# Kernel optimization log

Hardware: AMD Instinct MI355X
Metric: run time of the kernel (lower is better)

Reference implementation:

```python
import jax, jax.numpy as jnp
import numpy as np

N = 100000   # nodes
H = 96       # hidden_dim
A = 32       # attn_dim
De = 16      # edge_embeddings_dim
E = 500000   # edges per edge type
NEG_SLOPE = 0.01  # torch F.leaky_relu default


def setup_inputs() -> dict:
    key = jax.random.key(0)
    ks = jax.random.split(key, 24)
    nrm = lambda k, shape, s=1.0: jax.random.normal(k, shape, dtype=jnp.float32) * s
    idx = lambda k: jax.random.randint(k, (E,), 0, N, dtype=jnp.int32)
    Din = 2 * H + De
    return {
        'h': nrm(ks[0], (N, H)),
        'src0': idx(ks[1]), 'dst0': idx(ks[2]),
        'src1': idx(ks[3]), 'dst1': idx(ks[4]),
        'src2': idx(ks[5]), 'dst2': idx(ks[6]),
        'Wm0': nrm(ks[7], (Din, H), Din ** -0.5), 'bm0': jnp.zeros((H,), jnp.float32), 'ef0': nrm(ks[8], (De,)),
        'Wm1': nrm(ks[9], (Din, H), Din ** -0.5), 'bm1': jnp.zeros((H,), jnp.float32), 'ef1': nrm(ks[10], (De,)),
        'Wm2': nrm(ks[11], (Din, H), Din ** -0.5), 'bm2': jnp.zeros((H,), jnp.float32), 'ef2': nrm(ks[12], (De,)),
        'Wn0': nrm(ks[13], (H, A), H ** -0.5), 'Wa0': nrm(ks[14], (2 * A, 1), (2 * A) ** -0.5),
        'Wn1': nrm(ks[15], (H, A), H ** -0.5), 'Wa1': nrm(ks[16], (2 * A, 1), (2 * A) ** -0.5),
        'Wu': nrm(ks[17], (4 * H, H), (4 * H) ** -0.5), 'bu': jnp.zeros((H,), jnp.float32),
    }


def _leaky(x):
    return jnp.where(x > 0, x, NEG_SLOPE * x)


def _edge_msg(h, src, dst, Wm, bm, ef):
    # cat(src_h, dst_h, edge_feature) -> Linear  (dropout p=0, eval mode)
    x = jnp.concatenate([h[src], h[dst], jnp.broadcast_to(ef, (src.shape[0], ef.shape[0]))], axis=-1)
    return x @ Wm + bm  # [E, H]


def _mean_agg(m, dst):
    # fn.mean('m','msg'): per-destination mean over incoming edges
    s = jax.ops.segment_sum(m, dst, num_segments=N)
    c = jax.ops.segment_sum(jnp.ones((m.shape[0],), m.dtype), dst, num_segments=N)
    return s / jnp.maximum(c, 1.0)[:, None]


def _attn_agg(scores, m, dst):
    # per-destination softmax over mailbox (variable-size), then weighted sum
    smax = jax.ops.segment_max(scores, dst, num_segments=N)
    ex = jnp.exp(scores - smax[dst])
    den = jax.ops.segment_sum(ex, dst, num_segments=N)
    num = jax.ops.segment_sum(ex[:, None] * m, dst, num_segments=N)
    return num / jnp.maximum(den, 1e-9)[:, None]


def reference(h, src0, dst0, src1, dst1, src2, dst2,
              Wm0, bm0, ef0, Wm1, bm1, ef1, Wm2, bm2, ef2,
              Wn0, Wa0, Wn1, Wa1, Wu, bu):
    # edge type 0: intra_diff (attention), type 1: inter_diff (attention), type 2: intra_lt (mean)
    m0 = _edge_msg(h, src0, dst0, Wm0, bm0, ef0)
    m1 = _edge_msg(h, src1, dst1, Wm1, bm1, ef1)
    m2 = _edge_msg(h, src2, dst2, Wm2, bm2, ef2)

    z0 = h @ Wn0  # [N, A]
    s0 = _leaky(jnp.concatenate([z0[src0], z0[dst0]], axis=-1) @ Wa0)[:, 0]  # [E]
    z1 = h @ Wn1
    s1 = _leaky(jnp.concatenate([z1[src1], z1[dst1]], axis=-1) @ Wa1)[:, 0]

    msg0 = _attn_agg(s0, m0, dst0)   # [N, H]
    msg1 = _attn_agg(s1, m1, dst1)
    msg2 = _mean_agg(m2, dst2)

    # cross_reducer='stack' then concat over edge-type dim -> [N, 3H]
    mcat = jnp.concatenate([msg0, msg1, msg2], axis=-1)
    # cell node update: Linear(cat(h, m)) + ReLU
    return jax.nn.relu(jnp.concatenate([h, mcat], axis=-1) @ Wu + bu)
```

## Files before the change

### kernel.cpp

```cpp
#include <hip/hip_runtime.h>
#include <hip/hip_bf16.h>
#include <cstdint>

#define NN 100000
#define HH 96
#define AD 32
#define DE 16
#define EE 500000
#define NEG 0.01f

#define GSH 10
#define GSZ 1024
#define KB 98
#define CH 4096
#define BPT 123

typedef __bf16 bf16x8 __attribute__((ext_vector_type(8)));
typedef float  f32x4  __attribute__((ext_vector_type(4)));

__device__ __forceinline__ unsigned short f2b(float x) {
    union { float f; unsigned int u; } v; v.f = x;
    unsigned int r = v.u + 0x7fffu + ((v.u >> 16) & 1u);
    return (unsigned short)(r >> 16);
}
__device__ __forceinline__ float b2f(unsigned short h) {
    union { unsigned int u; float f; } v; v.u = ((unsigned int)h) << 16;
    return v.f;
}

__global__ void prep_kernel(const float* Wm0, const float* bm0, const float* ef0,
                            const float* Wm1, const float* bm1, const float* ef1,
                            const float* Wm2, const float* bm2, const float* ef2,
                            const float* Wn0, const float* Wa0,
                            const float* Wn1, const float* Wa1,
                            const float* Wu,
                            float* cvec, float* wvec,
                            unsigned short* BfN, unsigned short* BfU) {
    const float* Wm[3] = {Wm0, Wm1, Wm2};
    const float* bm[3] = {bm0, bm1, bm2};
    const float* ef[3] = {ef0, ef1, ef2};
    const int total = 288 + 384 + 55296 + 36864;
    for (int i = blockIdx.x * blockDim.x + threadIdx.x; i < total;
         i += gridDim.x * blockDim.x) {
        if (i < 288) {
            int t = i / 96, j = i % 96;
            float s = bm[t][j];
            for (int k = 0; k < DE; ++k) s += ef[t][k] * Wm[t][(2 * HH + k) * HH + j];
            cvec[i] = s;
        } else if (i < 288 + 384) {
            int ii = i - 288;
            int kind = ii / 96, k = ii % 96;
            const float* Wn = (kind < 2) ? Wn0 : Wn1;
            const float* Wa = (kind < 2) ? Wa0 : Wa1;
            int off = (kind & 1) ? AD : 0;
            float s = 0.f;
            for (int a = 0; a < AD; ++a) s += Wn[k * AD + a] * Wa[off + a];
            wvec[ii] = s;
        } else if (i < 288 + 384 + 55296) {
            int ii = i - 672;
            int sec = ii / 9216; int rem = ii % 9216;
            int ksc = rem / 512; int lj = rem % 512;
            int ks = ksc / 6, c = ksc % 6;
            int lane = lj / 8, jj = lj % 8;
            int quad = lane / 16, m = lane % 16;
            int k = ks * 32 + quad * 8 + jj;
            int n = c * 16 + m;
            int mt = (sec < 3) ? sec : sec - 3;
            int rowoff = (sec < 3) ? 0 : HH;
            BfN[ii] = f2b(Wm[mt][(rowoff + k) * HH + n]);
        } else {
            int ii = i - (672 + 55296);
            int ksc = ii / 512; int lj = ii % 512;
            int ks = ksc / 6, c = ksc % 6;
            int lane = lj / 8, jj = lj % 8;
            int quad = lane / 16, m = lane % 16;
            int k = ks * 32 + quad * 8 + jj;
            int n = c * 16 + m;
            BfU[ii] = f2b(Wu[k * HH + n]);
        }
    }
}

__global__ void cast_uv_kernel(const float* __restrict__ h, const float* __restrict__ wvec,
                               unsigned short* __restrict__ hb, float* __restrict__ uv) {
    int lane = threadIdx.x & 31;
    int node = (blockIdx.x * blockDim.x + threadIdx.x) >> 5;
    if (node >= NN) return;
    float h0 = h[node * HH + lane];
    float h1 = h[node * HH + 32 + lane];
    float h2 = h[node * HH + 64 + lane];
    hb[node * HH + lane] = f2b(h0);
    hb[node * HH + 32 + lane] = f2b(h1);
    hb[node * HH + 64 + lane] = f2b(h2);
    float acc[4];
#pragma unroll
    for (int q = 0; q < 4; ++q)
        acc[q] = h0 * wvec[q * 96 + lane] + h1 * wvec[q * 96 + 32 + lane] +
                 h2 * wvec[q * 96 + 64 + lane];
#pragma unroll
    for (int d = 16; d >= 1; d >>= 1)
#pragma unroll
        for (int q = 0; q < 4; ++q) acc[q] += __shfl_down(acc[q], d, 32);
    if (lane == 0) {
#pragma unroll
        for (int q = 0; q < 4; ++q) uv[q * NN + node] = acc[q];
    }
}

__global__ void zero_kernel(float4* __restrict__ p, int n4) {
    for (int i = blockIdx.x * blockDim.x + threadIdx.x; i < n4;
         i += gridDim.x * blockDim.x)
        p[i] = make_float4(0.f, 0.f, 0.f, 0.f);
}

__global__ void bucket_hist(const int* __restrict__ d0, const int* __restrict__ d1,
                            const int* __restrict__ d2, int* __restrict__ bCnt) {
    __shared__ int hist[3 * KB];
    int t = threadIdx.x;
    for (int j = t; j < 3 * KB; j += 256) hist[j] = 0;
    __syncthreads();
    const int total = 3 * EE;
    for (int i = blockIdx.x * blockDim.x + t; i < total; i += gridDim.x * blockDim.x) {
        int ty = i / EE, e = i - ty * EE;
        const int* d = (ty == 0) ? d0 : (ty == 1) ? d1 : d2;
        atomicAdd(&hist[ty * KB + (d[e] >> GSH)], 1);
    }
    __syncthreads();
    for (int j = t; j < 3 * KB; j += 256)
        if (hist[j]) atomicAdd(&bCnt[j], hist[j]);
}

__global__ void bucket_scan(const int* __restrict__ bCnt, int* __restrict__ bBase,
                            int* __restrict__ gCursor, int* __restrict__ rs) {
    __shared__ int hist[3 * KB];
    int t = threadIdx.x;
    if (t < 3 * KB) hist[t] = bCnt[t];
    __syncthreads();
    if (t < 3) {
        int run = 0;
        for (int b = 0; b < KB; ++b) {
            bBase[t * (KB + 1) + b] = run;
            gCursor[t * KB + b] = run;
            run += hist[t * KB + b];
        }
        bBase[t * (KB + 1) + KB] = run;
        rs[(size_t)t * (NN + 1) + NN] = run;
    }
}

__global__ __launch_bounds__(256) void bucket_scatter(
    const int* __restrict__ s0, const int* __restrict__ d0,
    const int* __restrict__ s1, const int* __restrict__ d1,
    const int* __restrict__ s2, const int* __restrict__ d2,
    int* __restrict__ gCursor, unsigned int* __restrict__ binned) {
    __shared__ unsigned int recs[CH];
    __shared__ unsigned short rnk[CH];
    __shared__ unsigned char bkt[CH];
    __shared__ int cnt[KB];
    __shared__ int gpos[KB];
    int t = threadIdx.x;
    int type = blockIdx.x / BPT;
    int chunk = (blockIdx.x % BPT) * CH;
    const int* src = (type == 0) ? s0 : (type == 1) ? s1 : s2;
    const int* dst = (type == 0) ? d0 : (type == 1) ? d1 : d2;
    if (t < KB) cnt[t] = 0;
    __syncthreads();
#pragma unroll
    for (int k = 0; k < CH / 256; ++k) {
        int idx = k * 256 + t;
        int e = chunk + idx;
        if (e < EE) {
            int s = src[e], d = dst[e];
            int b = d >> GSH;
            recs[idx] = ((unsigned int)s << GSH) | (unsigned int)(d & (GSZ - 1));
            bkt[idx] = (unsigned char)b;
            rnk[idx] = (unsigned short)atomicAdd(&cnt[b], 1);
        } else {
            bkt[idx] = 0xFF;
        }
    }
    __syncthreads();
    if (t < KB) {
        int c = cnt[t];
        gpos[t] = (c > 0) ? atomicAdd(&gCursor[type * KB + t], c) : 0;
    }
    __syncthreads();
    unsigned int* bout = binned + (size_t)type * EE;
#pragma unroll
    for (int k = 0; k < CH / 256; ++k) {
        int idx = k * 256 + t;
        unsigned char b = bkt[idx];
        if (b != 0xFF) bout[gpos[b] + rnk[idx]] = recs[idx];
    }
}

__global__ __launch_bounds__(256) void bucket_sort(
    const unsigned int* __restrict__ binned, const int* __restrict__ bBase,
    int* __restrict__ rs, int* __restrict__ sorted) {
    __shared__ int cnt[GSZ];
    __shared__ int tsum[256];
    int t = threadIdx.x;
    int type = blockIdx.x / KB;
    int b = blockIdx.x % KB;
    int nodeBase = b * GSZ;
    int eb = bBase[type * (KB + 1) + b];
    int en = bBase[type * (KB + 1) + b + 1];
    int n = en - eb;
    const unsigned int* bin = binned + (size_t)type * EE + eb;
#pragma unroll
    for (int k = 0; k < GSZ / 256; ++k) cnt[k * 256 + t] = 0;
    __syncthreads();
    for (int i = t; i < n; i += 256) atomicAdd(&cnt[bin[i] & (GSZ - 1)], 1);
    __syncthreads();
    int v[4], s = 0;
#pragma unroll
    for (int k = 0; k < 4; ++k) { v[k] = cnt[t * 4 + k]; s += v[k]; }
    tsum[t] = s;
    __syncthreads();
    for (int off = 1; off < 256; off <<= 1) {
        int add = (t >= off) ? tsum[t - off] : 0;
        __syncthreads();
        tsum[t] += add;
        __syncthreads();
    }
    int run = tsum[t] - s;
    int offk[4];
#pragma unroll
    for (int k = 0; k < 4; ++k) { offk[k] = run; run += v[k]; }
    int* rsrow = rs + (size_t)type * (NN + 1) + nodeBase;
#pragma unroll
    for (int k = 0; k < 4; ++k) {
        int node = t * 4 + k;
        if (nodeBase + node < NN) rsrow[node] = eb + offk[k];
    }
    __syncthreads();
#pragma unroll
    for (int k = 0; k < 4; ++k) cnt[t * 4 + k] = offk[k];
    __syncthreads();
    int* so = sorted + (size_t)type * EE + eb;
    for (int i = t; i < n; i += 256) {
        unsigned int r = bin[i];
        int dl = r & (GSZ - 1);
        int p = atomicAdd(&cnt[dl], 1);
        so[p] = (int)(r >> GSH);
    }
}

__global__ __launch_bounds__(256) void node_gemm_kernel(const unsigned short* __restrict__ hb,
                                                        const unsigned short* __restrict__ BfN,
                                                        unsigned short* __restrict__ Pall,
                                                        unsigned short* __restrict__ Qall) {
    const size_t NH = (size_t)NN * HH;
    int wave = threadIdx.x >> 6;
    int lane = threadIdx.x & 63;
    int quad = lane >> 4, m = lane & 15;
    int blk = blockIdx.x * 4 + wave;
    if (blk >= NN / 16) return;
    int sec = blockIdx.y;
    unsigned short* dst = (sec < 3) ? (Pall + (size_t)sec * NH)
                                    : (Qall + (size_t)(sec - 3) * NH);
    int r0 = blk * 16;
    f32x4 acc[6] = {};
    const unsigned short* arow = hb + (size_t)(r0 + m) * HH + quad * 8;
#pragma unroll
    for (int ks = 0; ks < 3; ++ks) {
        bf16x8 af = *(const bf16x8*)(arow + ks * 32);
#pragma unroll
        for (int c = 0; c < 6; ++c) {
            bf16x8 bfv = *(const bf16x8*)(BfN + (((sec * 3 + ks) * 6 + c) << 9) + lane * 8);
            acc[c] = __builtin_amdgcn_mfma_f32_16x16x32_bf16(af, bfv, acc[c], 0, 0, 0);
        }
    }
#pragma unroll
    for (int c = 0; c < 6; ++c)
#pragma unroll
        for (int r = 0; r < 4; ++r) {
            int row = r0 + quad * 4 + r;
            dst[(size_t)row * HH + c * 16 + m] = f2b(acc[c][r]);
        }
}

__global__ void aggregate_kernel(const int* __restrict__ rsAll, const int* __restrict__ sortedAll,
                                 const float* __restrict__ uv,
                                 const unsigned short* __restrict__ Pall,
                                 const unsigned short* __restrict__ Qall,
                                 const float* __restrict__ cvec,
                                 unsigned short* __restrict__ msgb) {
    const size_t NH = (size_t)NN * HH;
    int lane = threadIdx.x & 31;
    int node = (blockIdx.x * blockDim.x + threadIdx.x) >> 5;
    if (node >= NN) return;
    int t = blockIdx.y;
    int is_attn = (t < 2);
    const int* rs = rsAll + (size_t)t * (NN + 1);
    const int* sorted = sortedAll + (size_t)t * EE;
    const float* u = uv + 2 * t * NN;
    const unsigned short* P = Pall + (size_t)t * NH;
    const unsigned short* Q = Qall + (size_t)t * NH;
    const float* cvec_t = cvec + t * 96;

    int beg = rs[node], end = rs[node + 1];
    float a0 = 0.f, a1 = 0.f, a2 = 0.f, den = 0.f;
    float vd = is_attn ? uv[(2 * t + 1) * NN + node] : 0.f;
    for (int base = beg; base < end; base += 32) {
        int batch = end - base;
        if (batch > 32) batch = 32;
        int li = lane < batch ? lane : batch - 1;
        int myS = sorted[base + li];
#pragma unroll 1
        for (int j = 0; j < batch; j += 8) {
            int rem = batch - j;
            int sI[8];
            float wv[8];
#pragma unroll
            for (int k = 0; k < 8; ++k) sI[k] = __shfl(myS, (k < rem ? j + k : j), 32);
            if (is_attn) {
#pragma unroll
                for (int k = 0; k < 8; ++k) {
                    float c = u[sI[k]] + vd;
                    c = c > 0.f ? c : NEG * c;
                    wv[k] = __expf(c);
                }
            } else {
#pragma unroll
                for (int k = 0; k < 8; ++k) wv[k] = 1.f;
            }
#pragma unroll
            for (int k = 0; k < 8; ++k) if (k >= rem) wv[k] = 0.f;
            float x0[8], x1[8], x2[8];
#pragma unroll
            for (int k = 0; k < 8; ++k) {
                const unsigned short* pr = P + (size_t)sI[k] * HH;
                x0[k] = b2f(pr[lane]);
                x1[k] = b2f(pr[lane + 32]);
                x2[k] = b2f(pr[lane + 64]);
            }
#pragma unroll
            for (int k = 0; k < 8; ++k) {
                den += wv[k];
                a0 += wv[k] * x0[k];
                a1 += wv[k] * x1[k];
                a2 += wv[k] * x2[k];
            }
        }
    }
    float r0 = 0.f, r1 = 0.f, r2 = 0.f;
    if (den > 0.f) {
        float inv = 1.f / den;
        const unsigned short* qr = Q + (size_t)node * HH;
        r0 = a0 * inv + b2f(qr[lane]) + cvec_t[lane];
        r1 = a1 * inv + b2f(qr[lane + 32]) + cvec_t[lane + 32];
        r2 = a2 * inv + b2f(qr[lane + 64]) + cvec_t[lane + 64];
    }
    unsigned short* mr = msgb + (size_t)node * 288 + t * 96;
    mr[lane] = f2b(r0);
    mr[lane + 32] = f2b(r1);
    mr[lane + 64] = f2b(r2);
}

__global__ __launch_bounds__(256) void update_gemm_kernel(const unsigned short* __restrict__ hb,
                                                          const unsigned short* __restrict__ msgb,
                                                          const unsigned short* __restrict__ BfU,
                                                          const float* __restrict__ bu,
                                                          float* __restrict__ out) {
    int wave = threadIdx.x >> 6;
    int lane = threadIdx.x & 63;
    int quad = lane >> 4, m = lane & 15;
    int blk = blockIdx.x * 4 + wave;
    if (blk >= NN / 16) return;
    int r0 = blk * 16;
    f32x4 acc[6] = {};
#pragma unroll
    for (int ks = 0; ks < 12; ++ks) {
        const unsigned short* ap =
            (ks < 3) ? hb + (size_t)(r0 + m) * HH + ks * 32 + quad * 8
                     : msgb + (size_t)(r0 + m) * 288 + (ks - 3) * 32 + quad * 8;
        bf16x8 af = *(const bf16x8*)ap;
#pragma unroll
        for (int c = 0; c < 6; ++c) {
            bf16x8 bfv = *(const bf16x8*)(BfU + ((ks * 6 + c) << 9) + lane * 8);
            acc[c] = __builtin_amdgcn_mfma_f32_16x16x32_bf16(af, bfv, acc[c], 0, 0, 0);
        }
    }
#pragma unroll
    for (int c = 0; c < 6; ++c) {
        float b = bu[c * 16 + m];
#pragma unroll
        for (int r = 0; r < 4; ++r) {
            int row = r0 + quad * 4 + r;
            float v2 = acc[c][r] + b;
            out[(size_t)row * HH + c * 16 + m] = v2 > 0.f ? v2 : 0.f;
        }
    }
}

extern "C" void kernel_launch(void* const* d_in, const int* in_sizes, int n_in,
                              void* d_out, int out_size, void* d_ws, size_t ws_size,
                              hipStream_t stream) {
    (void)in_sizes; (void)n_in; (void)out_size;
    const float* h   = (const float*)d_in[0];
    const int* srcs[3] = {(const int*)d_in[1], (const int*)d_in[3], (const int*)d_in[5]};
    const int* dsts[3] = {(const int*)d_in[2], (const int*)d_in[4], (const int*)d_in[6]};
    const float* Wm0 = (const float*)d_in[7];
    const float* bm0 = (const float*)d_in[8];
    const float* ef0 = (const float*)d_in[9];
    const float* Wm1 = (const float*)d_in[10];
    const float* bm1 = (const float*)d_in[11];
    const float* ef1 = (const float*)d_in[12];
    const float* Wm2 = (const float*)d_in[13];
    const float* bm2 = (const float*)d_in[14];
    const float* ef2 = (const float*)d_in[15];
    const float* Wn0 = (const float*)d_in[16];
    const float* Wa0 = (const float*)d_in[17];
    const float* Wn1 = (const float*)d_in[18];
    const float* Wa1 = (const float*)d_in[19];
    const float* Wu  = (const float*)d_in[20];
    const float* bu  = (const float*)d_in[21];
    float* out = (float*)d_out;

    const size_t NEED = 206991104;
    if (ws_size < NEED) return;
    char* w = (char*)d_ws;
    unsigned short* msgb    = (unsigned short*)(w + 0);
    unsigned short* hb      = (unsigned short*)(w + 57600000);
    unsigned short* Pall    = (unsigned short*)(w + 76800000);
    unsigned short* Qall    = (unsigned short*)(w + 134400000);
    float*          uv      = (float*)(w + 192000000);
    float*          cvec    = (float*)(w + 193600000);
    float*          wvec    = (float*)(w + 193601280);
    unsigned short* BfN     = (unsigned short*)(w + 193602816);
    unsigned short* BfU     = (unsigned short*)(w + 193713408);
    int*            bBase   = (int*)(w + 193787136);
    int*            gCursor = (int*)(w + 193788416);
    int*            bCnt    = (int*)(w + 193789696);
    int*            rs      = (int*)(w + 193790976);
    int*            sorted  = (int*)(w + 194991104);
    unsigned int*   binned  = (unsigned int*)(w + 200991104);

    prep_kernel<<<128, 256, 0, stream>>>(Wm0, bm0, ef0, Wm1, bm1, ef1, Wm2, bm2, ef2,
                                         Wn0, Wa0, Wn1, Wa1, Wu, cvec, wvec, BfN, BfU);
    cast_uv_kernel<<<12500, 256, 0, stream>>>(h, wvec, hb, uv);

    zero_kernel<<<1, 256, 0, stream>>>((float4*)bCnt, 80);
    bucket_hist<<<512, 256, 0, stream>>>(dsts[0], dsts[1], dsts[2], bCnt);
    bucket_scan<<<1, 384, 0, stream>>>(bCnt, bBase, gCursor, rs);
    bucket_scatter<<<3 * BPT, 256, 0, stream>>>(srcs[0], dsts[0], srcs[1], dsts[1],
                                                srcs[2], dsts[2], gCursor, binned);
    bucket_sort<<<3 * KB, 256, 0, stream>>>(binned, bBase, rs, sorted);

    node_gemm_kernel<<<dim3(1563, 6), 256, 0, stream>>>(hb, BfN, Pall, Qall);
    aggregate_kernel<<<dim3(12500, 3), 256, 0, stream>>>(rs, sorted, uv, Pall, Qall,
                                                         cvec, msgb);
    update_gemm_kernel<<<1563, 256, 0, stream>>>(hb, msgb, BfU, bu, out);
}
```

Before: 346.9 us.

## Aggregate raw node features before projection, then apply message GEMM per node

Moves the linear message projection after the per-destination aggregation. The aggregate kernel now gathers rows of the shared bf16 h (one table for all three edge types) instead of three per-type projected P tables, and writes normalized aggregated h plus the denominator. A new GEMM kernel combines the aggregated h with the source weights and h with the destination weights, adds the bias/edge-feature constant, and zeros nodes with no incoming edges. This removes the separate P/Q precompute and cuts gather table size, which should improve cache hit rate, at the cost of an extra intermediate write/read of the aggregated features and slightly different bf16 rounding order.

```diff
diff --git a/kernel.cpp b/kernel.cpp
--- a/kernel.cpp
+++ b/kernel.cpp
@@ -246,46 +246,11 @@
     }
 }
 
-__global__ __launch_bounds__(256) void node_gemm_kernel(const unsigned short* __restrict__ hb,
-                                                        const unsigned short* __restrict__ BfN,
-                                                        unsigned short* __restrict__ Pall,
-                                                        unsigned short* __restrict__ Qall) {
-    const size_t NH = (size_t)NN * HH;
-    int wave = threadIdx.x >> 6;
-    int lane = threadIdx.x & 63;
-    int quad = lane >> 4, m = lane & 15;
-    int blk = blockIdx.x * 4 + wave;
-    if (blk >= NN / 16) return;
-    int sec = blockIdx.y;
-    unsigned short* dst = (sec < 3) ? (Pall + (size_t)sec * NH)
-                                    : (Qall + (size_t)(sec - 3) * NH);
-    int r0 = blk * 16;
-    f32x4 acc[6] = {};
-    const unsigned short* arow = hb + (size_t)(r0 + m) * HH + quad * 8;
-#pragma unroll
-    for (int ks = 0; ks < 3; ++ks) {
-        bf16x8 af = *(const bf16x8*)(arow + ks * 32);
-#pragma unroll
-        for (int c = 0; c < 6; ++c) {
-            bf16x8 bfv = *(const bf16x8*)(BfN + (((sec * 3 + ks) * 6 + c) << 9) + lane * 8);
-            acc[c] = __builtin_amdgcn_mfma_f32_16x16x32_bf16(af, bfv, acc[c], 0, 0, 0);
-        }
-    }
-#pragma unroll
-    for (int c = 0; c < 6; ++c)
-#pragma unroll
-        for (int r = 0; r < 4; ++r) {
-            int row = r0 + quad * 4 + r;
-            dst[(size_t)row * HH + c * 16 + m] = f2b(acc[c][r]);
-        }
-}
-
 __global__ void aggregate_kernel(const int* __restrict__ rsAll, const int* __restrict__ sortedAll,
                                  const float* __restrict__ uv,
-                                 const unsigned short* __restrict__ Pall,
-                                 const unsigned short* __restrict__ Qall,
-                                 const float* __restrict__ cvec,
-                                 unsigned short* __restrict__ msgb) {
+                                 const unsigned short* __restrict__ hb,
+                                 unsigned short* __restrict__ hagg,
+                                 float* __restrict__ den) {
     const size_t NH = (size_t)NN * HH;
     int lane = threadIdx.x & 31;
     int node = (blockIdx.x * blockDim.x + threadIdx.x) >> 5;
@@ -295,12 +260,9 @@
     const int* rs = rsAll + (size_t)t * (NN + 1);
     const int* sorted = sortedAll + (size_t)t * EE;
     const float* u = uv + 2 * t * NN;
-    const unsigned short* P = Pall + (size_t)t * NH;
-    const unsigned short* Q = Qall + (size_t)t * NH;
-    const float* cvec_t = cvec + t * 96;
 
     int beg = rs[node], end = rs[node + 1];
-    float a0 = 0.f, a1 = 0.f, a2 = 0.f, den = 0.f;
+    float a0 = 0.f, a1 = 0.f, a2 = 0.f, dn = 0.f;
     float vd = is_attn ? uv[(2 * t + 1) * NN + node] : 0.f;
     for (int base = beg; base < end; base += 32) {
         int batch = end - base;
@@ -330,14 +292,14 @@
             float x0[8], x1[8], x2[8];
 #pragma unroll
             for (int k = 0; k < 8; ++k) {
-                const unsigned short* pr = P + (size_t)sI[k] * HH;
+                const unsigned short* pr = hb + (size_t)sI[k] * HH;
                 x0[k] = b2f(pr[lane]);
                 x1[k] = b2f(pr[lane + 32]);
                 x2[k] = b2f(pr[lane + 64]);
             }
 #pragma unroll
             for (int k = 0; k < 8; ++k) {
-                den += wv[k];
+                dn += wv[k];
                 a0 += wv[k] * x0[k];
                 a1 += wv[k] * x1[k];
                 a2 += wv[k] * x2[k];
@@ -345,17 +307,60 @@
         }
     }
     float r0 = 0.f, r1 = 0.f, r2 = 0.f;
-    if (den > 0.f) {
-        float inv = 1.f / den;
-        const unsigned short* qr = Q + (size_t)node * HH;
-        r0 = a0 * inv + b2f(qr[lane]) + cvec_t[lane];
-        r1 = a1 * inv + b2f(qr[lane + 32]) + cvec_t[lane + 32];
-        r2 = a2 * inv + b2f(qr[lane + 64]) + cvec_t[lane + 64];
-    }
-    unsigned short* mr = msgb + (size_t)node * 288 + t * 96;
+    if (dn > 0.f) {
+        float inv = 1.f / dn;
+        r0 = a0 * inv; r1 = a1 * inv; r2 = a2 * inv;
+    }
+    unsigned short* mr = hagg + (size_t)t * NH + (size_t)node * HH;
     mr[lane] = f2b(r0);
     mr[lane + 32] = f2b(r1);
     mr[lane + 64] = f2b(r2);
+    if (lane == 0) den[(size_t)t * NN + node] = dn;
+}
+
+__global__ __launch_bounds__(256) void msg_gemm_kernel(const unsigned short* __restrict__ hagg,
+                                                       const unsigned short* __restrict__ hb,
+                                                       const unsigned short* __restrict__ BfN,
+                                                       const float* __restrict__ den,
+                                                       const float* __restrict__ cvec,
+                                                       unsigned short* __restrict__ msgb) {
+    const size_t NH = (size_t)NN * HH;
+    int wave = threadIdx.x >> 6;
+    int lane = threadIdx.x & 63;
+    int quad = lane >> 4, m = lane & 15;
+    int blk = blockIdx.x * 4 + wave;
+    if (blk >= NN / 16) return;
+    int t = blockIdx.y;
+    int r0 = blk * 16;
+    const unsigned short* ha = hagg + (size_t)t * NH;
+    f32x4 acc[6] = {};
+#pragma unroll
+    for (int ks = 0; ks < 6; ++ks) {
+        const unsigned short* ap =
+            (ks < 3) ? ha + (size_t)(r0 + m) * HH + ks * 32 + quad * 8
+                     : hb + (size_t)(r0 + m) * HH + (ks - 3) * 32 + quad * 8;
+        int sec = (ks < 3) ? t : t + 3;
+        int kk = (ks < 3) ? ks : ks - 3;
+        bf16x8 af = *(const bf16x8*)ap;
+#pragma unroll
+        for (int c = 0; c < 6; ++c) {
+            bf16x8 bfv = *(const bf16x8*)(BfN + (((sec * 3 + kk) * 6 + c) << 9) + lane * 8);
+            acc[c] = __builtin_amdgcn_mfma_f32_16x16x32_bf16(af, bfv, acc[c], 0, 0, 0);
+        }
+    }
+    float dn[4];
+#pragma unroll
+    for (int r = 0; r < 4; ++r) dn[r] = den[(size_t)t * NN + r0 + quad * 4 + r];
+#pragma unroll
+    for (int c = 0; c < 6; ++c) {
+        float cv = cvec[t * 96 + c * 16 + m];
+#pragma unroll
+        for (int r = 0; r < 4; ++r) {
+            int row = r0 + quad * 4 + r;
+            float val = (dn[r] > 0.f) ? (acc[c][r] + cv) : 0.f;
+            msgb[(size_t)row * 288 + t * 96 + c * 16 + m] = f2b(val);
+        }
+    }
 }
 
 __global__ __launch_bounds__(256) void update_gemm_kernel(const unsigned short* __restrict__ hb,
@@ -418,24 +423,24 @@
     const float* bu  = (const float*)d_in[21];
     float* out = (float*)d_out;
 
-    const size_t NEED = 206991104;
+    const size_t NEED = 150591104;
     if (ws_size < NEED) return;
     char* w = (char*)d_ws;
     unsigned short* msgb    = (unsigned short*)(w + 0);
     unsigned short* hb      = (unsigned short*)(w + 57600000);
-    unsigned short* Pall    = (unsigned short*)(w + 76800000);
-    unsigned short* Qall    = (unsigned short*)(w + 134400000);
-    float*          uv      = (float*)(w + 192000000);
-    float*          cvec    = (float*)(w + 193600000);
-    float*          wvec    = (float*)(w + 193601280);
-    unsigned short* BfN     = (unsigned short*)(w + 193602816);
-    unsigned short* BfU     = (unsigned short*)(w + 193713408);
-    int*            bBase   = (int*)(w + 193787136);
-    int*            gCursor = (int*)(w + 193788416);
-    int*            bCnt    = (int*)(w + 193789696);
-    int*            rs      = (int*)(w + 193790976);
-    int*            sorted  = (int*)(w + 194991104);
-    unsigned int*   binned  = (unsigned int*)(w + 200991104);
+    unsigned short* hagg    = (unsigned short*)(w + 76800000);
+    float*          den     = (float*)(w + 134400000);
+    float*          uv      = (float*)(w + 135600000);
+    float*          cvec    = (float*)(w + 137200000);
+    float*          wvec    = (float*)(w + 137201280);
+    unsigned short* BfN     = (unsigned short*)(w + 137202816);
+    unsigned short* BfU     = (unsigned short*)(w + 137313408);
+    int*            bBase   = (int*)(w + 137387136);
+    int*            gCursor = (int*)(w + 137388416);
+    int*            bCnt    = (int*)(w + 137389696);
+    int*            rs      = (int*)(w + 137390976);
+    int*            sorted  = (int*)(w + 138591104);
+    unsigned int*   binned  = (unsigned int*)(w + 144591104);
 
     prep_kernel<<<128, 256, 0, stream>>>(Wm0, bm0, ef0, Wm1, bm1, ef1, Wm2, bm2, ef2,
                                          Wn0, Wa0, Wn1, Wa1, Wu, cvec, wvec, BfN, BfU);
@@ -448,8 +453,7 @@
                                                 srcs[2], dsts[2], gCursor, binned);
     bucket_sort<<<3 * KB, 256, 0, stream>>>(binned, bBase, rs, sorted);
 
-    node_gemm_kernel<<<dim3(1563, 6), 256, 0, stream>>>(hb, BfN, Pall, Qall);
-    aggregate_kernel<<<dim3(12500, 3), 256, 0, stream>>>(rs, sorted, uv, Pall, Qall,
-                                                         cvec, msgb);
+    aggregate_kernel<<<dim3(12500, 3), 256, 0, stream>>>(rs, sorted, uv, hb, hagg, den);
+    msg_gemm_kernel<<<dim3(1563, 3), 256, 0, stream>>>(hagg, hb, BfN, den, cvec, msgb);
     update_gemm_kernel<<<1563, 256, 0, stream>>>(hb, msgb, BfU, bu, out);
 }
```

New measurement: 331.5 us. 4.5% less time.
